# Performance work log

Measured on AMD Instinct MI355X. Metric: run time of the kernel, lower is better.

Reference implementation:

```python
import jax, jax.numpy as jnp
import numpy as np

N = 100000   # nodes
E = 1600000  # edges (pos and neg each)
F_IN = 256
H = 64       # hidden == out_dim


def setup_inputs() -> dict:
    key = jax.random.key(0)
    ks = jax.random.split(key, 12)
    x = jax.random.normal(ks[0], (N, F_IN), dtype=jnp.float32)
    edge_index = jax.random.randint(ks[1], (2, E), 0, N, dtype=jnp.int64)
    neg_edge_index = jax.random.randint(ks[2], (2, E), 0, N, dtype=jnp.int64)
    s = 0.05
    return {
        "x": x,
        "edge_index": edge_index,
        "neg_edge_index": neg_edge_index,
        "W1": jax.random.normal(ks[3], (F_IN, H), dtype=jnp.float32) * s,
        "b1": jnp.zeros((H,), jnp.float32),
        "W2": jax.random.normal(ks[4], (H, H), dtype=jnp.float32) * s,
        "b2": jnp.zeros((H,), jnp.float32),
        "Wp1": jax.random.normal(ks[5], (2 * H, 128), dtype=jnp.float32) * s,
        "bp1": jnp.zeros((128,), jnp.float32),
        "Wp2": jax.random.normal(ks[6], (128, 64), dtype=jnp.float32) * s,
        "bp2": jnp.zeros((64,), jnp.float32),
        "Wp3": jax.random.normal(ks[7], (64, 1), dtype=jnp.float32) * s,
        "bp3": jnp.zeros((1,), jnp.float32),
    }


def gcn_conv(x, edge_index, W, b):
    # PyG GCNConv: add self-loops, symmetric normalization D^-1/2 (A+I) D^-1/2, x@W + b
    xw = x @ W  # [N,H]
    loop = jnp.arange(N, dtype=edge_index.dtype)
    src = jnp.concatenate([edge_index[0], loop])
    dst = jnp.concatenate([edge_index[1], loop])
    deg = jax.ops.segment_sum(jnp.ones(src.shape[0], xw.dtype), dst, num_segments=N)
    dinv = jnp.where(deg > 0, jax.lax.rsqrt(jnp.maximum(deg, 1e-12)), 0.0)
    norm = dinv[src] * dinv[dst]  # [E+N]
    msgs = xw[src] * norm[:, None]
    out = jax.ops.segment_sum(msgs, dst, num_segments=N)
    return out + b


def predict_link(z, edge_index, Wp1, bp1, Wp2, bp2, Wp3, bp3):
    src, dst = edge_index[0], edge_index[1]
    # cat([z[src], z[dst]]) @ Wp1 == z[src] @ Wp1[:H] + z[dst] @ Wp1[H:]
    h = jnp.maximum(z[src] @ Wp1[:H] + z[dst] @ Wp1[H:] + bp1, 0.0)
    h = jnp.maximum(h @ Wp2 + bp2, 0.0)
    return (h @ Wp3 + bp3)[:, 0]


def reference(x, edge_index, neg_edge_index, W1, b1, W2, b2, Wp1, bp1, Wp2, bp2, Wp3, bp3):
    # encode (dropout inactive: eval mode)
    z = jnp.maximum(gcn_conv(x, edge_index, W1, b1), 0.0)
    z = jnp.maximum(gcn_conv(z, edge_index, W2, b2), 0.0)
    pos = predict_link(z, edge_index, Wp1, bp1, Wp2, bp2, Wp3, bp3)
    neg = predict_link(z, neg_edge_index, Wp1, bp1, Wp2, bp2, Wp3, bp3)
    return pos, neg, z
```

## Files before the change

kernel.cpp:

```cpp
#include <hip/hip_runtime.h>

#define NODES 100000
#define SCAN_B 200
#define CHUNK 500

typedef __attribute__((ext_vector_type(4))) float f4v;
typedef __attribute__((ext_vector_type(8))) short bfx8;
typedef __attribute__((ext_vector_type(4))) float f32x4;
typedef __attribute__((ext_vector_type(4))) unsigned short us4v;
typedef __attribute__((ext_vector_type(2))) unsigned int u2v;
typedef unsigned short ushort_t;
typedef unsigned int uint_t;

__device__ __forceinline__ ushort_t f2b(float f) {
  union { float f; uint_t u; } v; v.f = f;
  return (ushort_t)((v.u + 0x7fffu + ((v.u >> 16) & 1u)) >> 16);
}
__device__ __forceinline__ float b2f(ushort_t h) {
  union { uint_t u; float f; } v; v.u = ((uint_t)h) << 16;
  return v.f;
}

#define MFMA16(A, B, C) __builtin_amdgcn_mfma_f32_16x16x32_bf16((A), (B), (C), 0, 0, 0)


__global__ void count_deg(const int* __restrict__ dst, int* __restrict__ deg, int E) {
  int i = blockIdx.x * 256 + threadIdx.x;
  if (i < E) atomicAdd(&deg[dst[i]], 1);
}

__global__ void dinv_k(const int* __restrict__ deg, float* __restrict__ dinv, int n) {
  int i = blockIdx.x * 256 + threadIdx.x;
  if (i < n) dinv[i] = 1.0f / sqrtf((float)(deg[i] + 1));
}

__global__ void scan_sum(const int* __restrict__ deg, int* __restrict__ bsum) {
  __shared__ int sh[256];
  int b = blockIdx.x, t = threadIdx.x;
  int base = b * CHUNK;
  int v = 0;
  for (int i = t; i < CHUNK; i += 256) v += deg[base + i];
  sh[t] = v;
  __syncthreads();
  for (int s = 128; s > 0; s >>= 1) {
    if (t < s) sh[t] += sh[t + s];
    __syncthreads();
  }
  if (t == 0) bsum[b] = sh[0];
}

__global__ void scan_top(int* __restrict__ bsum) {
  __shared__ int sh[SCAN_B];
  int t = threadIdx.x;
  if (t < SCAN_B) sh[t] = bsum[t];
  __syncthreads();
  if (t == 0) {
    int run = 0;
    for (int i = 0; i < SCAN_B; ++i) { int x = sh[i]; sh[i] = run; run += x; }
  }
  __syncthreads();
  if (t < SCAN_B) bsum[t] = sh[t];
}

__global__ void scan_out(const int* __restrict__ deg, const int* __restrict__ bsum,
                         int* __restrict__ row_start, int E) {
  __shared__ int sh[CHUNK];
  int b = blockIdx.x, t = threadIdx.x;
  int base = b * CHUNK;
  for (int i = t; i < CHUNK; i += 256) sh[i] = deg[base + i];
  __syncthreads();
  if (t == 0) {
    int run = bsum[b];
    for (int i = 0; i < CHUNK; ++i) { int x = sh[i]; sh[i] = run; run += x; }
  }
  __syncthreads();
  for (int i = t; i < CHUNK; i += 256) row_start[base + i] = sh[i];
  if (b == SCAN_B - 1 && t == 0) row_start[NODES] = E;
}

__global__ void fill_csr(const int* __restrict__ src, const int* __restrict__ dst,
                         const int* __restrict__ row_start, int* __restrict__ cursor,
                         int* __restrict__ csr, int E) {
  int i = blockIdx.x * 256 + threadIdx.x;
  if (i < E) {
    int d = dst[i];
    int p = atomicAdd(&cursor[d], 1);
    csr[row_start[d] + p] = src[i];
  }
}

template <int K>
__global__ __launch_bounds__(256) void conv_gemm(
    const float* __restrict__ A, const float* __restrict__ W,
    const float* __restrict__ dinv, float* __restrict__ out, int n) {
  constexpr int KT = K / 32;
  constexpr int SEGS = K / 8;
  __shared__ __align__(16) ushort_t lhi[32 * K];
  __shared__ __align__(16) ushort_t llo[32 * K];

  int tid = threadIdx.x;
  int lane = tid & 63, wave = tid >> 6;
  int q = lane & 15, g = lane >> 4;
  int c0 = wave * 16;
  int r0 = blockIdx.x * 32;

  bfx8 bhi[KT], blo[KT];
#pragma unroll
  for (int kt = 0; kt < KT; ++kt) {
    bfx8 h, l;
#pragma unroll
    for (int j = 0; j < 8; ++j) {
      float w = W[(size_t)(kt * 32 + g * 8 + j) * 64 + c0 + q];
      ushort_t hb = f2b(w);
      float lo = w - b2f(hb);
      h[j] = (short)hb;
      l[j] = (short)f2b(lo);
    }
    bhi[kt] = h;
    blo[kt] = l;
  }

  for (int idx = tid; idx < 32 * SEGS; idx += 256) {
    int row = idx / SEGS, s = idx % SEGS;
    const float* p = A + (size_t)(r0 + row) * K + s * 8;
    f4v v0 = *(const f4v*)p;
    f4v v1 = *(const f4v*)(p + 4);
    bfx8 h8, l8;
#pragma unroll
    for (int j = 0; j < 4; ++j) {
      ushort_t hb = f2b(v0[j]);
      h8[j] = (short)hb;
      l8[j] = (short)f2b(v0[j] - b2f(hb));
      ushort_t hb1 = f2b(v1[j]);
      h8[4 + j] = (short)hb1;
      l8[4 + j] = (short)f2b(v1[j] - b2f(hb1));
    }
    int boff = row * (K * 2) + ((s * 16) ^ ((row & 7) << 4));
    *(bfx8*)((char*)lhi + boff) = h8;
    *(bfx8*)((char*)llo + boff) = l8;
  }
  __syncthreads();

  f32x4 hh[2], hl[2], lh[2];
#pragma unroll
  for (int rt = 0; rt < 2; ++rt) {
    hh[rt] = (f32x4){0.f, 0.f, 0.f, 0.f};
    hl[rt] = (f32x4){0.f, 0.f, 0.f, 0.f};
    lh[rt] = (f32x4){0.f, 0.f, 0.f, 0.f};
  }
#pragma unroll
  for (int kt = 0; kt < KT; ++kt) {
#pragma unroll
    for (int rt = 0; rt < 2; ++rt) {
      int row = rt * 16 + q;
      int boff = row * (K * 2) + (((kt * 64 + g * 16)) ^ ((row & 7) << 4));
      bfx8 ah = *(const bfx8*)((const char*)lhi + boff);
      bfx8 al = *(const bfx8*)((const char*)llo + boff);
      hh[rt] = MFMA16(ah, bhi[kt], hh[rt]);
      hl[rt] = MFMA16(ah, blo[kt], hl[rt]);
      lh[rt] = MFMA16(al, bhi[kt], lh[rt]);
    }
  }

#pragma unroll
  for (int rt = 0; rt < 2; ++rt) {
    f32x4 s = hh[rt] + hl[rt] + lh[rt];
#pragma unroll
    for (int j = 0; j < 4; ++j) {
      int row = r0 + rt * 16 + g * 4 + j;
      if (row < n) out[(size_t)row * 64 + c0 + q] = s[j] * dinv[row];
    }
  }
}

__global__ void agg_k(const float* __restrict__ P, const int* __restrict__ row_start,
                      const int* __restrict__ csr, const float* __restrict__ dinv,
                      const float* __restrict__ bias, float* __restrict__ out,
                      ushort_t* __restrict__ zb, int n) {
  int wave = threadIdx.x >> 6, lane = threadIdx.x & 63;
  int i = blockIdx.x * 4 + wave;
  if (i >= n) return;
  const float* Pl = P + lane;
  float a0 = Pl[(size_t)i * 64];
  float a1 = 0.f, a2 = 0.f, a3 = 0.f;
  int beg = row_start[i], end = row_start[i + 1];
  int j = beg;
  for (; j + 8 <= end; j += 8) {
    int s0 = csr[j + 0], s1 = csr[j + 1], s2 = csr[j + 2], s3 = csr[j + 3];
    int s4 = csr[j + 4], s5 = csr[j + 5], s6 = csr[j + 6], s7 = csr[j + 7];
    float v0 = Pl[(size_t)s0 * 64];
    float v1 = Pl[(size_t)s1 * 64];
    float v2 = Pl[(size_t)s2 * 64];
    float v3 = Pl[(size_t)s3 * 64];
    float v4 = Pl[(size_t)s4 * 64];
    float v5 = Pl[(size_t)s5 * 64];
    float v6 = Pl[(size_t)s6 * 64];
    float v7 = Pl[(size_t)s7 * 64];
    a0 += v0; a1 += v1; a2 += v2; a3 += v3;
    a0 += v4; a1 += v5; a2 += v6; a3 += v7;
  }
  if (j + 4 <= end) {
    int s0 = csr[j + 0], s1 = csr[j + 1], s2 = csr[j + 2], s3 = csr[j + 3];
    float v0 = Pl[(size_t)s0 * 64];
    float v1 = Pl[(size_t)s1 * 64];
    float v2 = Pl[(size_t)s2 * 64];
    float v3 = Pl[(size_t)s3 * 64];
    a0 += v0; a1 += v1; a2 += v2; a3 += v3;
    j += 4;
  }
  for (; j < end; ++j) a1 += Pl[(size_t)csr[j] * 64];
  float acc = (a0 + a1) + (a2 + a3);
  float v = fmaxf(acc * dinv[i] + bias[lane], 0.0f);
  out[(size_t)i * 64 + lane] = v;
  if (zb) zb[(size_t)i * 64 + lane] = f2b(v);
}

__global__ __launch_bounds__(256, 2) void mlp_kernel(
    const int* __restrict__ ei, const ushort_t* __restrict__ zb,
    const float* __restrict__ Wp1, const float* __restrict__ bp1,
    const float* __restrict__ Wp2, const float* __restrict__ bp2,
    const float* __restrict__ Wp3, const float* __restrict__ bp3,
    float* __restrict__ out, int E) {
  __shared__ __align__(16) char WT1[32768];
  __shared__ __align__(16) char H1[4][8192];

  int tid = threadIdx.x;
  for (int idx = tid; idx < 128 * 128; idx += 256) {
    int k = idx >> 7, n = idx & 127;
    int boff = n * 256 + (((k * 2) ^ ((n & 7) << 4)));
    *(ushort_t*)(WT1 + boff) = f2b(Wp1[idx]);
  }
  __syncthreads();

  int lane = tid & 63, wave = tid >> 6;
  int q = lane & 15, g = lane >> 4;
  char* H1w = &H1[wave][0];

  bfx8 wf2r[16];
#pragma unroll
  for (int t2 = 0; t2 < 4; ++t2)
#pragma unroll
    for (int kk = 0; kk < 4; ++kk) {
      bfx8 v;
#pragma unroll
      for (int j = 0; j < 8; ++j) {
        int k = kk * 32 + g * 8 + j;
        int n = t2 * 16 + q;
        v[j] = (short)f2b(Wp2[k * 64 + n]);
      }
      wf2r[t2 * 4 + kk] = v;
    }
  float b1r[32], b2r[16], w3r[16];
#pragma unroll
  for (int t = 0; t < 8; ++t)
#pragma unroll
    for (int j = 0; j < 4; ++j) b1r[t * 4 + j] = bp1[t * 16 + g * 4 + j];
#pragma unroll
  for (int t = 0; t < 4; ++t)
#pragma unroll
    for (int j = 0; j < 4; ++j) {
      b2r[t * 4 + j] = bp2[t * 16 + g * 4 + j];
      w3r[t * 4 + j] = Wp3[t * 16 + g * 4 + j];
    }
  float bp3v = bp3[0];

  int ntile = E >> 7;
  for (int tile = blockIdx.x; tile < ntile; tile += gridDim.x) {
    int ebase = (tile << 7) + (wave << 5);

    bfx8 af[2][4];
#pragma unroll
    for (int eb = 0; eb < 2; ++eb) {
      int e = ebase + eb * 16 + q;
      int s = ei[e], d = ei[E + e];
#pragma unroll
      for (int kk = 0; kk < 4; ++kk) {
        int node = (kk < 2) ? s : d;
        int off = ((kk & 1) << 5) + (g << 3);
        af[eb][kk] = *(const bfx8*)(zb + (size_t)node * 64 + off);
      }
    }

#pragma unroll
    for (int t = 0; t < 8; ++t) {
      f32x4 acc1[2];
      acc1[0] = (f32x4){0.f, 0.f, 0.f, 0.f};
      acc1[1] = (f32x4){0.f, 0.f, 0.f, 0.f};
#pragma unroll
      for (int kk = 0; kk < 4; ++kk) {
        int n = t * 16 + q;
        bfx8 wf = *(const bfx8*)(WT1 + n * 256 + (((kk * 64 + g * 16)) ^ ((n & 7) << 4)));
        acc1[0] = MFMA16(wf, af[0][kk], acc1[0]);
        acc1[1] = MFMA16(wf, af[1][kk], acc1[1]);
      }
#pragma unroll
      for (int eb = 0; eb < 2; ++eb) {
        float v0 = fmaxf(acc1[eb][0] + b1r[t * 4 + 0], 0.f);
        float v1 = fmaxf(acc1[eb][1] + b1r[t * 4 + 1], 0.f);
        float v2 = fmaxf(acc1[eb][2] + b1r[t * 4 + 2], 0.f);
        float v3 = fmaxf(acc1[eb][3] + b1r[t * 4 + 3], 0.f);
        u2v pk;
        pk[0] = (uint_t)f2b(v0) | ((uint_t)f2b(v1) << 16);
        pk[1] = (uint_t)f2b(v2) | ((uint_t)f2b(v3) << 16);
        int row = eb * 16 + q;
        int bcol = ((t * 32 + g * 8)) ^ ((row & 7) << 4);
        *(u2v*)(H1w + row * 256 + bcol) = pk;
      }
    }
    asm volatile("s_waitcnt lgkmcnt(0)" ::: "memory");

#pragma unroll
    for (int eb = 0; eb < 2; ++eb) {
      f32x4 acc2[4];
#pragma unroll
      for (int t2 = 0; t2 < 4; ++t2) acc2[t2] = (f32x4){0.f, 0.f, 0.f, 0.f};
#pragma unroll
      for (int kk = 0; kk < 4; ++kk) {
        int row = eb * 16 + q;
        bfx8 hf = *(const bfx8*)(H1w + row * 256 + (((kk * 64 + g * 16)) ^ ((row & 7) << 4)));
#pragma unroll
        for (int t2 = 0; t2 < 4; ++t2) acc2[t2] = MFMA16(wf2r[t2 * 4 + kk], hf, acc2[t2]);
      }
      float sacc = 0.f;
#pragma unroll
      for (int t2 = 0; t2 < 4; ++t2)
#pragma unroll
        for (int j = 0; j < 4; ++j) {
          float h = fmaxf(acc2[t2][j] + b2r[t2 * 4 + j], 0.f);
          sacc += h * w3r[t2 * 4 + j];
        }
      sacc += __shfl_xor(sacc, 16);
      sacc += __shfl_xor(sacc, 32);
      if (g == 0) out[ebase + eb * 16 + q] = sacc + bp3v;
    }
  }
}


static inline size_t alup(size_t x) { return (x + 511) & ~(size_t)511; }

extern "C" void kernel_launch(void* const* d_in, const int* in_sizes, int n_in,
                              void* d_out, int out_size, void* d_ws, size_t ws_size,
                              hipStream_t stream) {
  const float* x = (const float*)d_in[0];
  const int* ei = (const int*)d_in[1];
  const int* nei = (const int*)d_in[2];
  const float* W1 = (const float*)d_in[3];
  const float* b1 = (const float*)d_in[4];
  const float* W2 = (const float*)d_in[5];
  const float* b2 = (const float*)d_in[6];
  const float* Wp1 = (const float*)d_in[7];
  const float* bp1 = (const float*)d_in[8];
  const float* Wp2 = (const float*)d_in[9];
  const float* bp2 = (const float*)d_in[10];
  const float* Wp3 = (const float*)d_in[11];
  const float* bp3 = (const float*)d_in[12];

  const int N = NODES;
  const int E = in_sizes[1] / 2;

  float* pos = (float*)d_out;
  float* neg = pos + E;
  float* z = pos + (size_t)2 * E;

  char* w = (char*)d_ws;
  size_t off = 0;
  int* deg = (int*)(w + off); off = alup(off + (size_t)N * 4);
  int* cur = (int*)(w + off); off = alup(off + (size_t)N * 4);
  float* dinv = (float*)(w + off); off = alup(off + (size_t)N * 4);
  int* bsum = (int*)(w + off); off = alup(off + 256 * 4);
  int* row_start = (int*)(w + off); off = alup(off + (size_t)(N + 1) * 4);
  int* csr = (int*)(w + off); off = alup(off + (size_t)E * 4);
  float* xw = (float*)(w + off); off = alup(off + (size_t)N * 64 * 4);
  float* z1 = (float*)(w + off); off = alup(off + (size_t)N * 64 * 4);
  ushort_t* zb = (ushort_t*)(w + off); off = alup(off + (size_t)N * 64 * 2);

  hipMemsetAsync(deg, 0, (size_t)N * 4, stream);
  hipMemsetAsync(cur, 0, (size_t)N * 4, stream);

  count_deg<<<(E + 255) / 256, 256, 0, stream>>>(ei + E, deg, E);
  dinv_k<<<(N + 255) / 256, 256, 0, stream>>>(deg, dinv, N);
  scan_sum<<<SCAN_B, 256, 0, stream>>>(deg, bsum);
  scan_top<<<1, 256, 0, stream>>>(bsum);
  scan_out<<<SCAN_B, 256, 0, stream>>>(deg, bsum, row_start, E);
  fill_csr<<<(E + 255) / 256, 256, 0, stream>>>(ei, ei + E, row_start, cur, csr, E);

  conv_gemm<256><<<(N + 31) / 32, 256, 0, stream>>>(x, W1, dinv, xw, N);
  agg_k<<<(N + 3) / 4, 256, 0, stream>>>(xw, row_start, csr, dinv, b1, z1, nullptr, N);
  conv_gemm<64><<<(N + 31) / 32, 256, 0, stream>>>(z1, W2, dinv, xw, N);
  agg_k<<<(N + 3) / 4, 256, 0, stream>>>(xw, row_start, csr, dinv, b2, z, zb, N);

  mlp_kernel<<<1024, 256, 0, stream>>>(ei, zb, Wp1, bp1, Wp2, bp2, Wp3, bp3, pos, E);
  mlp_kernel<<<1024, 256, 0, stream>>>(nei, zb, Wp1, bp1, Wp2, bp2, Wp3, bp3, neg, E);
}
```

Baseline: 566.6 us.

## Chain MLP layers in registers via permuted Wp1 and lane shuffles, dropping LDS staging

Removes the per-wave LDS staging buffer for the first MLP layer's output. Wp1 columns and bp1 are permuted so that each MFMA accumulator tile, after a few xor lane shuffles, lines up directly with the B-operand layout of the second-layer MFMA, which is now interleaved with the first layer. Biases and Wp3 move from per-thread registers into small LDS arrays, launch bounds rise to 3 blocks per CU, and the grid grows to cover all tiles. The intent is to cut LDS round-trips and register pressure so occupancy can rise; the cost is shuffle traffic and fragile permutation logic.

```diff
diff --git a/kernel.cpp b/kernel.cpp
--- a/kernel.cpp
+++ b/kernel.cpp
@@ -1,4 +1,5 @@
 #include <hip/hip_runtime.h>
+#include <hip/hip_bf16.h>
 
 #define NODES 100000
 #define SCAN_B 200
@@ -8,7 +9,6 @@
 typedef __attribute__((ext_vector_type(8))) short bfx8;
 typedef __attribute__((ext_vector_type(4))) float f32x4;
 typedef __attribute__((ext_vector_type(4))) unsigned short us4v;
-typedef __attribute__((ext_vector_type(2))) unsigned int u2v;
 typedef unsigned short ushort_t;
 typedef unsigned int uint_t;
 
@@ -19,6 +19,18 @@
 __device__ __forceinline__ float b2f(ushort_t h) {
   union { uint_t u; float f; } v; v.u = ((uint_t)h) << 16;
   return v.f;
+}
+__device__ __forceinline__ uint_t pk2(float a, float b) {
+  union { __hip_bfloat16 h; ushort_t u; } lo, hi;
+  lo.h = __float2bfloat16(a);
+  hi.h = __float2bfloat16(b);
+  return (uint_t)lo.u | ((uint_t)hi.u << 16);
+}
+
+__device__ __forceinline__ int permn1(int r) {
+  int t = r >> 4, g = (r >> 2) & 3, p = (r >> 1) & 1, e = r & 1;
+  int w = 2 * (t & 1) + p;
+  return 32 * (t >> 1) + 8 * (g ^ w) + 2 * w + e;
 }
 
 #define MFMA16(A, B, C) __builtin_amdgcn_mfma_f32_16x16x32_bf16((A), (B), (C), 0, 0, 0)
@@ -215,26 +227,29 @@
   if (zb) zb[(size_t)i * 64 + lane] = f2b(v);
 }
 
-__global__ __launch_bounds__(256, 2) void mlp_kernel(
+__global__ __launch_bounds__(256, 3) void mlp_kernel(
     const int* __restrict__ ei, const ushort_t* __restrict__ zb,
     const float* __restrict__ Wp1, const float* __restrict__ bp1,
     const float* __restrict__ Wp2, const float* __restrict__ bp2,
     const float* __restrict__ Wp3, const float* __restrict__ bp3,
     float* __restrict__ out, int E) {
   __shared__ __align__(16) char WT1[32768];
-  __shared__ __align__(16) char H1[4][8192];
+  __shared__ __align__(16) float Lb1[128];
+  __shared__ __align__(16) float Lb2[64];
+  __shared__ __align__(16) float Lw3[64];
 
   int tid = threadIdx.x;
   for (int idx = tid; idx < 128 * 128; idx += 256) {
-    int k = idx >> 7, n = idx & 127;
-    int boff = n * 256 + (((k * 2) ^ ((n & 7) << 4)));
-    *(ushort_t*)(WT1 + boff) = f2b(Wp1[idx]);
-  }
+    int k = idx >> 7, r = idx & 127;
+    int boff = r * 256 + ((k * 2) ^ ((r & 7) << 4));
+    *(ushort_t*)(WT1 + boff) = f2b(Wp1[k * 128 + permn1(r)]);
+  }
+  if (tid < 128) Lb1[tid] = bp1[permn1(tid)];
+  if (tid < 64) { Lb2[tid] = bp2[tid]; Lw3[tid] = Wp3[tid]; }
   __syncthreads();
 
   int lane = tid & 63, wave = tid >> 6;
   int q = lane & 15, g = lane >> 4;
-  char* H1w = &H1[wave][0];
 
   bfx8 wf2r[16];
 #pragma unroll
@@ -243,24 +258,9 @@
     for (int kk = 0; kk < 4; ++kk) {
       bfx8 v;
 #pragma unroll
-      for (int j = 0; j < 8; ++j) {
-        int k = kk * 32 + g * 8 + j;
-        int n = t2 * 16 + q;
-        v[j] = (short)f2b(Wp2[k * 64 + n]);
-      }
+      for (int j = 0; j < 8; ++j)
+        v[j] = (short)f2b(Wp2[(kk * 32 + g * 8 + j) * 64 + t2 * 16 + q]);
       wf2r[t2 * 4 + kk] = v;
-    }
-  float b1r[32], b2r[16], w3r[16];
-#pragma unroll
-  for (int t = 0; t < 8; ++t)
-#pragma unroll
-    for (int j = 0; j < 4; ++j) b1r[t * 4 + j] = bp1[t * 16 + g * 4 + j];
-#pragma unroll
-  for (int t = 0; t < 4; ++t)
-#pragma unroll
-    for (int j = 0; j < 4; ++j) {
-      b2r[t * 4 + j] = bp2[t * 16 + g * 4 + j];
-      w3r[t * 4 + j] = Wp3[t * 16 + g * 4 + j];
     }
   float bp3v = bp3[0];
 
@@ -281,56 +281,64 @@
       }
     }
 
-#pragma unroll
-    for (int t = 0; t < 8; ++t) {
-      f32x4 acc1[2];
-      acc1[0] = (f32x4){0.f, 0.f, 0.f, 0.f};
-      acc1[1] = (f32x4){0.f, 0.f, 0.f, 0.f};
+    f32x4 acc2[2][4];
+#pragma unroll
+    for (int eb = 0; eb < 2; ++eb)
+#pragma unroll
+      for (int t2 = 0; t2 < 4; ++t2) acc2[eb][t2] = (f32x4){0.f, 0.f, 0.f, 0.f};
+
+#pragma unroll
+    for (int m = 0; m < 4; ++m) {
+      int t0 = 2 * m, t1 = 2 * m + 1;
+      f32x4 a0[2], a1[2];
+      a0[0] = (f32x4){0.f, 0.f, 0.f, 0.f};
+      a0[1] = (f32x4){0.f, 0.f, 0.f, 0.f};
+      a1[0] = (f32x4){0.f, 0.f, 0.f, 0.f};
+      a1[1] = (f32x4){0.f, 0.f, 0.f, 0.f};
 #pragma unroll
       for (int kk = 0; kk < 4; ++kk) {
-        int n = t * 16 + q;
-        bfx8 wf = *(const bfx8*)(WT1 + n * 256 + (((kk * 64 + g * 16)) ^ ((n & 7) << 4)));
-        acc1[0] = MFMA16(wf, af[0][kk], acc1[0]);
-        acc1[1] = MFMA16(wf, af[1][kk], acc1[1]);
+        int n0 = t0 * 16 + q, n1 = t1 * 16 + q;
+        bfx8 wf0 = *(const bfx8*)(WT1 + n0 * 256 + (((kk * 64 + g * 16)) ^ ((n0 & 7) << 4)));
+        bfx8 wf1 = *(const bfx8*)(WT1 + n1 * 256 + (((kk * 64 + g * 16)) ^ ((n1 & 7) << 4)));
+        a0[0] = MFMA16(wf0, af[0][kk], a0[0]);
+        a0[1] = MFMA16(wf0, af[1][kk], a0[1]);
+        a1[0] = MFMA16(wf1, af[0][kk], a1[0]);
+        a1[1] = MFMA16(wf1, af[1][kk], a1[1]);
       }
+      f4v bv0 = *(const f4v*)(Lb1 + t0 * 16 + g * 4);
+      f4v bv1 = *(const f4v*)(Lb1 + t1 * 16 + g * 4);
 #pragma unroll
       for (int eb = 0; eb < 2; ++eb) {
-        float v0 = fmaxf(acc1[eb][0] + b1r[t * 4 + 0], 0.f);
-        float v1 = fmaxf(acc1[eb][1] + b1r[t * 4 + 1], 0.f);
-        float v2 = fmaxf(acc1[eb][2] + b1r[t * 4 + 2], 0.f);
-        float v3 = fmaxf(acc1[eb][3] + b1r[t * 4 + 3], 0.f);
-        u2v pk;
-        pk[0] = (uint_t)f2b(v0) | ((uint_t)f2b(v1) << 16);
-        pk[1] = (uint_t)f2b(v2) | ((uint_t)f2b(v3) << 16);
-        int row = eb * 16 + q;
-        int bcol = ((t * 32 + g * 8)) ^ ((row & 7) << 4);
-        *(u2v*)(H1w + row * 256 + bcol) = pk;
+        uint_t c0 = pk2(fmaxf(a0[eb][0] + bv0[0], 0.f), fmaxf(a0[eb][1] + bv0[1], 0.f));
+        uint_t c1 = pk2(fmaxf(a0[eb][2] + bv0[2], 0.f), fmaxf(a0[eb][3] + bv0[3], 0.f));
+        uint_t c2 = pk2(fmaxf(a1[eb][0] + bv1[0], 0.f), fmaxf(a1[eb][1] + bv1[1], 0.f));
+        uint_t c3 = pk2(fmaxf(a1[eb][2] + bv1[2], 0.f), fmaxf(a1[eb][3] + bv1[3], 0.f));
+        uint_t d1 = __shfl_xor(c1, 16, 64);
+        uint_t d2 = __shfl_xor(c2, 32, 64);
+        uint_t d3 = __shfl_xor(c3, 48, 64);
+        union { uint_t u[4]; bfx8 v; } hf;
+        hf.u[0] = c0; hf.u[1] = d1; hf.u[2] = d2; hf.u[3] = d3;
+#pragma unroll
+        for (int t2 = 0; t2 < 4; ++t2)
+          acc2[eb][t2] = MFMA16(wf2r[t2 * 4 + m], hf.v, acc2[eb][t2]);
       }
     }
-    asm volatile("s_waitcnt lgkmcnt(0)" ::: "memory");
 
 #pragma unroll
     for (int eb = 0; eb < 2; ++eb) {
-      f32x4 acc2[4];
-#pragma unroll
-      for (int t2 = 0; t2 < 4; ++t2) acc2[t2] = (f32x4){0.f, 0.f, 0.f, 0.f};
-#pragma unroll
-      for (int kk = 0; kk < 4; ++kk) {
-        int row = eb * 16 + q;
-        bfx8 hf = *(const bfx8*)(H1w + row * 256 + (((kk * 64 + g * 16)) ^ ((row & 7) << 4)));
-#pragma unroll
-        for (int t2 = 0; t2 < 4; ++t2) acc2[t2] = MFMA16(wf2r[t2 * 4 + kk], hf, acc2[t2]);
+      float sacc = 0.f;
+#pragma unroll
+      for (int t2 = 0; t2 < 4; ++t2) {
+        f4v b2v = *(const f4v*)(Lb2 + t2 * 16 + g * 4);
+        f4v w3v = *(const f4v*)(Lw3 + t2 * 16 + g * 4);
+#pragma unroll
+        for (int j = 0; j < 4; ++j) {
+          float h = fmaxf(acc2[eb][t2][j] + b2v[j], 0.f);
+          sacc = fmaf(h, w3v[j], sacc);
+        }
       }
-      float sacc = 0.f;
-#pragma unroll
-      for (int t2 = 0; t2 < 4; ++t2)
-#pragma unroll
-        for (int j = 0; j < 4; ++j) {
-          float h = fmaxf(acc2[t2][j] + b2r[t2 * 4 + j], 0.f);
-          sacc += h * w3r[t2 * 4 + j];
-        }
-      sacc += __shfl_xor(sacc, 16);
-      sacc += __shfl_xor(sacc, 32);
+      sacc += __shfl_xor(sacc, 16, 64);
+      sacc += __shfl_xor(sacc, 32, 64);
       if (g == 0) out[ebase + eb * 16 + q] = sacc + bp3v;
     }
   }
@@ -390,6 +398,8 @@
   conv_gemm<64><<<(N + 31) / 32, 256, 0, stream>>>(z1, W2, dinv, xw, N);
   agg_k<<<(N + 3) / 4, 256, 0, stream>>>(xw, row_start, csr, dinv, b2, z, zb, N);
 
-  mlp_kernel<<<1024, 256, 0, stream>>>(ei, zb, Wp1, bp1, Wp2, bp2, Wp3, bp3, pos, E);
-  mlp_kernel<<<1024, 256, 0, stream>>>(nei, zb, Wp1, bp1, Wp2, bp2, Wp3, bp3, neg, E);
-}
+  int ntile = E >> 7;
+  int grid = (ntile + 3) / 4;
+  mlp_kernel<<<grid, 256, 0, stream>>>(ei, zb, Wp1, bp1, Wp2, bp2, Wp3, bp3, pos, E);
+  mlp_kernel<<<grid, 256, 0, stream>>>(nei, zb, Wp1, bp1, Wp2, bp2, Wp3, bp3, neg, E);
+}
```

Result: slower. 1.746 ms (+208.1%).
